# Optimization experiments

Measured on AMD Instinct MI355X. Metric: run time of the kernel, lower is better.

## Reference

```python
import jax, jax.numpy as jnp
import numpy as np

HEADS = 16


def fenwick_mask(T):
    # Boolean [T, T] mask: diagonal + Fenwick-tree lookback positions, causal.
    m = np.zeros((T, T), dtype=bool)
    for i in range(T):
        j = i + 1
        while j <= T:
            m[i, j - 1] = True
            j += j & -j
        step = 1
        while i - step >= 0:
            m[i, i - step] = True
            step *= 2
    m &= np.tril(np.ones((T, T), dtype=bool))  # causal
    return jnp.asarray(m)


def setup_inputs() -> dict:
    key = jax.random.key(0)
    ks = jax.random.split(key, 4)
    B, T, C = 2, 2048, 1024
    x = jax.random.normal(ks[0], (B, T, C), dtype=jnp.float32)
    W_qkv = jax.random.normal(ks[1], (C, 3 * C), dtype=jnp.float32) * (C ** -0.5)
    b_qkv = jnp.zeros((3 * C,), dtype=jnp.float32)
    W_proj = jax.random.normal(ks[2], (C, C), dtype=jnp.float32) * (C ** -0.5)
    b_proj = jnp.zeros((C,), dtype=jnp.float32)
    return {"x": x, "W_qkv": W_qkv, "b_qkv": b_qkv, "W_proj": W_proj, "b_proj": b_proj}


def reference(x, W_qkv, b_qkv, W_proj, b_proj):
    B, T, C = x.shape
    H = HEADS
    Dh = C // H
    scale = Dh ** -0.5
    qkv = (x @ W_qkv + b_qkv).reshape(B, T, 3, H, Dh)
    qkv = jnp.transpose(qkv, (2, 0, 3, 1, 4))  # [3, B, H, T, Dh]
    q, k, v = qkv[0], qkv[1], qkv[2]
    attn = jnp.einsum('bhtd,bhsd->bhts', q, k) * scale  # [B, H, T, T]
    mask = fenwick_mask(T)  # trace-time constant
    attn = jnp.where(mask[None, None], attn, -jnp.inf)
    attn = jax.nn.softmax(attn, axis=-1)
    out = jnp.einsum('bhts,bhsd->bhtd', attn, v)  # [B, H, T, Dh]
    out = jnp.transpose(out, (0, 2, 1, 3)).reshape(B, T, C)
    return out @ W_proj + b_proj
```

## Files before the change

kernel.cpp:

```cpp
#include <hip/hip_runtime.h>
#include <hip/hip_bf16.h>


typedef unsigned short ushort_t;
typedef __attribute__((ext_vector_type(8))) short s16x8;
typedef __attribute__((ext_vector_type(4))) float f32x4;

#define T_SEQ 2048
#define C_DIM 1024
#define HEADS 16

__device__ __forceinline__ ushort_t f2bf(float f) {
    union { float f; unsigned u; } v{f};
    unsigned r = v.u + 0x7FFFu + ((v.u >> 16) & 1u);
    return (ushort_t)(r >> 16);
}
__device__ __forceinline__ float bf2f(ushort_t u) {
    union { unsigned u; float f; } v{((unsigned)u) << 16};
    return v.f;
}

__device__ __forceinline__ void async16(const ushort_t* g, ushort_t* l) {
    __builtin_amdgcn_global_load_lds(
        (const __attribute__((address_space(1))) void*)g,
        (__attribute__((address_space(3))) void*)l, 16, 0, 0);
}

__global__ void prep(const float* __restrict__ x, ushort_t* __restrict__ xb,
                     const float* __restrict__ Wq, ushort_t* __restrict__ WqT,
                     const float* __restrict__ Wp, ushort_t* __restrict__ WpT) {
    const int bid = blockIdx.x;
    const int tid = threadIdx.x;
    if (bid < 4096) {
        const int i = bid * 256 + tid;
        float4 f = ((const float4*)x)[i];
        ushort4 o;
        o.x = f2bf(f.x); o.y = f2bf(f.y); o.z = f2bf(f.z); o.w = f2bf(f.w);
        ((ushort4*)xb)[i] = o;
    } else {
        __shared__ ushort_t tile[32][33];
        const float* W; ushort_t* WT; int N, nb, kb;
        if (bid < 7168) {
            const int tb = bid - 4096;
            W = Wq; WT = WqT; N = 3072; nb = (tb % 96) * 32; kb = (tb / 96) * 32;
        } else {
            const int tb = bid - 7168;
            W = Wp; WT = WpT; N = 1024; nb = (tb & 31) * 32; kb = (tb >> 5) * 32;
        }
        const int tx = tid & 31, ty = tid >> 5;
        #pragma unroll
        for (int i = ty; i < 32; i += 8)
            tile[i][tx] = f2bf(W[(size_t)(kb + i) * N + nb + tx]);
        __syncthreads();
        #pragma unroll
        for (int i = ty; i < 32; i += 8)
            WT[(size_t)(nb + i) * 1024 + kb + tx] = tile[tx][i];
    }
}

__global__ void gemm_qkv(const ushort_t* __restrict__ A, const ushort_t* __restrict__ BT,
                         const float* __restrict__ bias, ushort_t* __restrict__ C,
                         int N, int K) {
    __shared__ ushort_t lsA[128 * 64];
    __shared__ ushort_t lsB[128 * 64];

    const int tid  = threadIdx.x;
    const int wave = tid >> 6;
    const int lane = tid & 63;
    const int row0 = blockIdx.x * 128;
    const int col0 = blockIdx.y * 128;
    const int wr   = (wave >> 1) * 64;
    const int wc   = (wave & 1) * 64;
    const int lrow = lane & 15;
    const int quad = lane >> 4;
    const int crow = lane >> 3;
    const int gcol = ((lane & 7) ^ crow) * 8;
    const int d3   = lrow & 7;

    f32x4 acc[4][4] = {};

    for (int k0 = 0; k0 < K; k0 += 64) {
        #pragma unroll
        for (int it = 0; it < 4; ++it) {
            const int chunk = it * 4 + wave;
            const int r = chunk * 8 + crow;
            async16(A  + (size_t)(row0 + r) * K + (k0 + gcol), lsA + chunk * 512);
            async16(BT + (size_t)(col0 + r) * K + (k0 + gcol), lsB + chunk * 512);
        }
        __syncthreads();
        #pragma unroll
        for (int kk = 0; kk < 64; kk += 32) {
            const int g = (kk >> 3) + quad;
            const int slot = (g ^ d3) << 3;
            s16x8 af[4], bfr[4];
            #pragma unroll
            for (int i = 0; i < 4; ++i)
                af[i] = *(const s16x8*)(lsA + (wr + i * 16 + lrow) * 64 + slot);
            #pragma unroll
            for (int j = 0; j < 4; ++j)
                bfr[j] = *(const s16x8*)(lsB + (wc + j * 16 + lrow) * 64 + slot);
            #pragma unroll
            for (int i = 0; i < 4; ++i)
                #pragma unroll
                for (int j = 0; j < 4; ++j)
                    acc[i][j] = __builtin_amdgcn_mfma_f32_16x16x32_bf16(
                        af[i], bfr[j], acc[i][j], 0, 0, 0);
        }
        __syncthreads();
    }

    #pragma unroll
    for (int i = 0; i < 4; ++i) {
        #pragma unroll
        for (int j = 0; j < 4; ++j) {
            const int col = col0 + wc + j * 16 + lrow;
            const float bv = bias[col];
            #pragma unroll
            for (int r = 0; r < 4; ++r) {
                const int row = row0 + wr + i * 16 + quad * 4 + r;
                C[(size_t)row * N + col] = f2bf(acc[i][j][r] + bv);
            }
        }
    }
}

__global__ void gemm_proj(const ushort_t* __restrict__ A, const ushort_t* __restrict__ BT,
                          const float* __restrict__ bias, float* __restrict__ C,
                          int N, int K) {
    __shared__ ushort_t lsA[128 * 64];
    __shared__ ushort_t lsB[64 * 64];

    const int tid  = threadIdx.x;
    const int wave = tid >> 6;
    const int lane = tid & 63;
    const int row0 = blockIdx.x * 128;
    const int col0 = blockIdx.y * 64;
    const int lrow = lane & 15;
    const int quad = lane >> 4;
    const int crow = lane >> 3;
    const int gcol = ((lane & 7) ^ crow) * 8;
    const int d3   = lrow & 7;

    f32x4 acc[2][4] = {};

    for (int k0 = 0; k0 < K; k0 += 64) {
        #pragma unroll
        for (int it = 0; it < 4; ++it) {
            const int chunk = it * 4 + wave;
            const int r = chunk * 8 + crow;
            async16(A + (size_t)(row0 + r) * K + (k0 + gcol), lsA + chunk * 512);
        }
        #pragma unroll
        for (int it = 0; it < 2; ++it) {
            const int chunk = it * 4 + wave;
            const int r = chunk * 8 + crow;
            async16(BT + (size_t)(col0 + r) * K + (k0 + gcol), lsB + chunk * 512);
        }
        __syncthreads();
        #pragma unroll
        for (int kk = 0; kk < 64; kk += 32) {
            const int g = (kk >> 3) + quad;
            const int slot = (g ^ d3) << 3;
            s16x8 af[2], bfr[4];
            #pragma unroll
            for (int i = 0; i < 2; ++i)
                af[i] = *(const s16x8*)(lsA + (wave * 32 + i * 16 + lrow) * 64 + slot);
            #pragma unroll
            for (int j = 0; j < 4; ++j)
                bfr[j] = *(const s16x8*)(lsB + (j * 16 + lrow) * 64 + slot);
            #pragma unroll
            for (int i = 0; i < 2; ++i)
                #pragma unroll
                for (int j = 0; j < 4; ++j)
                    acc[i][j] = __builtin_amdgcn_mfma_f32_16x16x32_bf16(
                        af[i], bfr[j], acc[i][j], 0, 0, 0);
        }
        __syncthreads();
    }

    #pragma unroll
    for (int i = 0; i < 2; ++i) {
        #pragma unroll
        for (int j = 0; j < 4; ++j) {
            const int col = col0 + j * 16 + lrow;
            const float bv = bias[col];
            #pragma unroll
            for (int r = 0; r < 4; ++r) {
                const int row = row0 + wave * 32 + i * 16 + quad * 4 + r;
                C[(size_t)row * N + col] = acc[i][j][r] + bv;
            }
        }
    }
}

__global__ void fenwick_attn(const ushort_t* __restrict__ QKV, ushort_t* __restrict__ AO) {
    const int lane = threadIdx.x & 63;
    const int wid  = blockIdx.x * 4 + (threadIdx.x >> 6);
    const int tile = wid & 255;
    const int bh   = wid >> 8;
    const int h    = bh & (HEADS - 1);
    const int b    = bh >> 4;
    const int tl   = lane >> 3;
    const int g    = lane & 7;
    const int t    = tile * 8 + tl;

    const ushort_t* base = QKV + (size_t)(b * T_SEQ) * 3072 + h * 64 + g * 8;

    float qf[8];
    {
        s16x8 qv = *(const s16x8*)(base + (size_t)t * 3072);
        #pragma unroll
        for (int e = 0; e < 8; ++e) qf[e] = bf2f((ushort_t)qv[e]);
    }

    float logit[12];
    int   pos[12];
    float mx = -1e30f;
    #pragma unroll
    for (int s = 0; s < 12; ++s) {
        const int step = (s == 0) ? 0 : (1 << (s - 1));
        const bool act = (step <= t);
        const int p = act ? (t - step) : t;
        pos[s] = p;
        s16x8 kv = *(const s16x8*)(base + (size_t)p * 3072 + 1024);
        float l = 0.f;
        #pragma unroll
        for (int e = 0; e < 8; ++e) l = fmaf(qf[e], bf2f((ushort_t)kv[e]), l);
        l += __shfl_xor(l, 1, 64);
        l += __shfl_xor(l, 2, 64);
        l += __shfl_xor(l, 4, 64);
        l *= 0.125f;
        logit[s] = act ? l : -1e30f;
        mx = fmaxf(mx, logit[s]);
    }

    float denom = 0.f;
    float ov[8] = {};
    #pragma unroll
    for (int s = 0; s < 12; ++s) {
        const float w = __expf(logit[s] - mx);
        denom += w;
        s16x8 vv = *(const s16x8*)(base + (size_t)pos[s] * 3072 + 2048);
        #pragma unroll
        for (int e = 0; e < 8; ++e) ov[e] = fmaf(w, bf2f((ushort_t)vv[e]), ov[e]);
    }

    const float inv = 1.f / denom;
    s16x8 os;
    #pragma unroll
    for (int e = 0; e < 8; ++e) os[e] = (short)f2bf(ov[e] * inv);
    *(s16x8*)(AO + (size_t)(b * T_SEQ + t) * C_DIM + h * 64 + g * 8) = os;
}

extern "C" void kernel_launch(void* const* d_in, const int* in_sizes, int n_in,
                              void* d_out, int out_size, void* d_ws, size_t ws_size,
                              hipStream_t stream) {
    const float* x      = (const float*)d_in[0];
    const float* W_qkv  = (const float*)d_in[1];
    const float* b_qkv  = (const float*)d_in[2];
    const float* W_proj = (const float*)d_in[3];
    const float* b_proj = (const float*)d_in[4];
    float* out = (float*)d_out;

    char* ws = (char*)d_ws;
    ushort_t* xb     = (ushort_t*)(ws);
    ushort_t* WqkvT  = (ushort_t*)(ws + (size_t)8  * 1048576);
    ushort_t* QKVb   = (ushort_t*)(ws + (size_t)14 * 1048576);
    ushort_t* AO     = (ushort_t*)(ws + (size_t)38 * 1048576);
    ushort_t* WprojT = (ushort_t*)(ws + (size_t)46 * 1048576);

    prep<<<8192, 256, 0, stream>>>(x, xb, W_qkv, WqkvT, W_proj, WprojT);
    gemm_qkv<<<dim3(32, 24), 256, 0, stream>>>(xb, WqkvT, b_qkv, QKVb, 3072, 1024);
    fenwick_attn<<<2048, 256, 0, stream>>>(QKVb, AO);
    gemm_proj<<<dim3(32, 16), 256, 0, stream>>>(AO, WprojT, b_proj, out, 1024, 1024);
}
```

Before: 150.0 us.

## Rewrite QKV GEMM as 256x192 tile with double-buffered async LDS pipeline

Replaces the 128x128 single-buffered QKV GEMM with a 512-thread, 256x192 tile kernel. Global-to-LDS async loads for the next K tiles are interleaved with MFMA phases across two LDS buffers, using explicit vmcnt waits, barriers and raised priority during MFMA. This is meant to hide load latency and raise data reuse per tile. It uses 112 KB of LDS and a larger accumulator set, and gives a 256-block grid that may fill the CUs less evenly.

```diff
diff --git a/kernel.cpp b/kernel.cpp
--- a/kernel.cpp
+++ b/kernel.cpp
@@ -58,66 +58,110 @@
     }
 }
 
-__global__ void gemm_qkv(const ushort_t* __restrict__ A, const ushort_t* __restrict__ BT,
-                         const float* __restrict__ bias, ushort_t* __restrict__ C,
-                         int N, int K) {
-    __shared__ ushort_t lsA[128 * 64];
-    __shared__ ushort_t lsB[128 * 64];
+
+#define BAR()  do { __builtin_amdgcn_sched_barrier(0); __builtin_amdgcn_s_barrier(); \
+                    __builtin_amdgcn_sched_barrier(0); } while (0)
+#define WAIT_LGKM0() do { asm volatile("s_waitcnt lgkmcnt(0)" ::: "memory"); \
+                          __builtin_amdgcn_sched_barrier(0); } while (0)
+#define WAIT_VM(n)  asm volatile("s_waitcnt vmcnt(" #n ")" ::: "memory")
+
+#define SA(kt, u, dst) async16(Ag + (size_t)(u) * rstep + (size_t)(kt) * 64, \
+                               (dst) + (u) * 4096 + wave * 512)
+#define SB(kt, u, dst) async16(Bg + (size_t)(u) * rstep + (size_t)(kt) * 64, \
+                               (dst) + (u) * 4096 + wave * 512)
+
+#define LDA_FRAG(buf, i, kh) (*(const s16x8*)((buf) + ((wm << 7) + (i) * 16 + lrow) * 64 \
+                               + ((((kh) * 4 + quad) ^ d3) << 3)))
+#define LDB_FRAG(buf, j, kh) (*(const s16x8*)((buf) + (wn * 48 + (j) * 16 + lrow) * 64 \
+                               + ((((kh) * 4 + quad) ^ d3) << 3)))
+
+#define PHASE(lAb, lBb, Q, LOADB, STAGES, ENDWAIT)                              \
+  {                                                                             \
+    s16x8 af[2][2];                                                             \
+    _Pragma("unroll") for (int ii = 0; ii < 2; ++ii)                            \
+      _Pragma("unroll") for (int kh = 0; kh < 2; ++kh)                          \
+        af[ii][kh] = LDA_FRAG(lAb, 2 * (Q) + ii, kh);                           \
+    if (LOADB) {                                                                \
+      _Pragma("unroll") for (int j = 0; j < 3; ++j)                             \
+        _Pragma("unroll") for (int kh = 0; kh < 2; ++kh)                        \
+          bf[j][kh] = LDB_FRAG(lBb, j, kh);                                     \
+    }                                                                           \
+    STAGES;                                                                     \
+    BAR();                                                                      \
+    WAIT_LGKM0();                                                               \
+    __builtin_amdgcn_s_setprio(1);                                              \
+    _Pragma("unroll") for (int ii = 0; ii < 2; ++ii)                            \
+      _Pragma("unroll") for (int j = 0; j < 3; ++j)                             \
+        _Pragma("unroll") for (int kh = 0; kh < 2; ++kh)                        \
+          acc[2 * (Q) + ii][j] = __builtin_amdgcn_mfma_f32_16x16x32_bf16(       \
+              af[ii][kh], bf[j][kh], acc[2 * (Q) + ii][j], 0, 0, 0);            \
+    __builtin_amdgcn_s_setprio(0);                                              \
+    ENDWAIT;                                                                    \
+    BAR();                                                                      \
+  }
+
+__global__ __launch_bounds__(512, 2)
+void gemm_qkv(const ushort_t* __restrict__ A, const ushort_t* __restrict__ BT,
+              const float* __restrict__ bias, ushort_t* __restrict__ C,
+              int N, int K) {
+    __shared__ ushort_t lds[57344];
 
     const int tid  = threadIdx.x;
     const int wave = tid >> 6;
     const int lane = tid & 63;
-    const int row0 = blockIdx.x * 128;
-    const int col0 = blockIdx.y * 128;
-    const int wr   = (wave >> 1) * 64;
-    const int wc   = (wave & 1) * 64;
+    const int wm   = wave >> 2;
+    const int wn   = wave & 3;
     const int lrow = lane & 15;
     const int quad = lane >> 4;
+    const int d3   = lrow & 7;
     const int crow = lane >> 3;
-    const int gcol = ((lane & 7) ^ crow) * 8;
-    const int d3   = lrow & 7;
-
-    f32x4 acc[4][4] = {};
-
-    for (int k0 = 0; k0 < K; k0 += 64) {
-        #pragma unroll
-        for (int it = 0; it < 4; ++it) {
-            const int chunk = it * 4 + wave;
-            const int r = chunk * 8 + crow;
-            async16(A  + (size_t)(row0 + r) * K + (k0 + gcol), lsA + chunk * 512);
-            async16(BT + (size_t)(col0 + r) * K + (k0 + gcol), lsB + chunk * 512);
-        }
-        __syncthreads();
-        #pragma unroll
-        for (int kk = 0; kk < 64; kk += 32) {
-            const int g = (kk >> 3) + quad;
-            const int slot = (g ^ d3) << 3;
-            s16x8 af[4], bfr[4];
-            #pragma unroll
-            for (int i = 0; i < 4; ++i)
-                af[i] = *(const s16x8*)(lsA + (wr + i * 16 + lrow) * 64 + slot);
-            #pragma unroll
-            for (int j = 0; j < 4; ++j)
-                bfr[j] = *(const s16x8*)(lsB + (wc + j * 16 + lrow) * 64 + slot);
-            #pragma unroll
-            for (int i = 0; i < 4; ++i)
-                #pragma unroll
-                for (int j = 0; j < 4; ++j)
-                    acc[i][j] = __builtin_amdgcn_mfma_f32_16x16x32_bf16(
-                        af[i], bfr[j], acc[i][j], 0, 0, 0);
-        }
-        __syncthreads();
-    }
-
-    #pragma unroll
-    for (int i = 0; i < 4; ++i) {
-        #pragma unroll
-        for (int j = 0; j < 4; ++j) {
-            const int col = col0 + wc + j * 16 + lrow;
+    const int gcol = (((lane & 7) ^ crow) << 3);
+    const int row0 = blockIdx.x * 256;
+    const int col0 = blockIdx.y * 192;
+
+    ushort_t* const lA0 = lds;
+    ushort_t* const lB0 = lds + 16384;
+    ushort_t* const lA1 = lds + 28672;
+    ushort_t* const lB1 = lds + 45056;
+
+    const ushort_t* Ag = A  + (size_t)(row0 + wave * 8 + crow) * K + gcol;
+    const ushort_t* Bg = BT + (size_t)(col0 + wave * 8 + crow) * K + gcol;
+    const size_t rstep = (size_t)64 * K;
+
+    f32x4 acc[8][3] = {};
+    s16x8 bf[3][2];
+
+    SA(0, 0, lA0); SA(0, 1, lA0); SA(0, 2, lA0); SA(0, 3, lA0);
+    SB(0, 0, lB0); SB(0, 1, lB0); SB(0, 2, lB0);
+    SB(1, 0, lB1); SB(1, 1, lB1); SA(1, 0, lA1); SA(1, 2, lA1); SB(1, 2, lB1);
+    WAIT_VM(5);
+    BAR();
+
+    const int nt = K >> 6;
+    for (int t = 0; t < nt; t += 2) {
+        const bool s2 = (t + 2) < nt;
+        const bool s3 = (t + 3) < nt;
+        PHASE(lA0, lB0, 0, true,  { SA(t + 1, 1, lA1); SA(t + 1, 3, lA1); }, {});
+        PHASE(lA0, lB0, 1, false, { if (s2) { SB(t + 2, 0, lB0); SB(t + 2, 1, lB0); } }, {});
+        PHASE(lA0, lB0, 2, false, { if (s2) { SA(t + 2, 0, lA0); SA(t + 2, 2, lA0); } }, {});
+        PHASE(lA0, lB0, 3, false, { if (s2) { SB(t + 2, 2, lB0); } },
+              { if (s2) { WAIT_VM(5); } else { WAIT_VM(0); } });
+        PHASE(lA1, lB1, 0, true,  { if (s2) { SA(t + 2, 1, lA0); SA(t + 2, 3, lA0); } }, {});
+        PHASE(lA1, lB1, 1, false, { if (s3) { SB(t + 3, 0, lB1); SB(t + 3, 1, lB1); } }, {});
+        PHASE(lA1, lB1, 2, false, { if (s3) { SA(t + 3, 0, lA1); SA(t + 3, 2, lA1); } }, {});
+        PHASE(lA1, lB1, 3, false, { if (s3) { SB(t + 3, 2, lB1); } },
+              { WAIT_VM(5); });
+    }
+
+    #pragma unroll
+    for (int i = 0; i < 8; ++i) {
+        #pragma unroll
+        for (int j = 0; j < 3; ++j) {
+            const int col = col0 + wn * 48 + j * 16 + lrow;
             const float bv = bias[col];
             #pragma unroll
             for (int r = 0; r < 4; ++r) {
-                const int row = row0 + wr + i * 16 + quad * 4 + r;
+                const int row = row0 + (wm << 7) + i * 16 + quad * 4 + r;
                 C[(size_t)row * N + col] = f2bf(acc[i][j][r] + bv);
             }
         }
@@ -270,7 +314,7 @@
     ushort_t* WprojT = (ushort_t*)(ws + (size_t)46 * 1048576);
 
     prep<<<8192, 256, 0, stream>>>(x, xb, W_qkv, WqkvT, W_proj, WprojT);
-    gemm_qkv<<<dim3(32, 24), 256, 0, stream>>>(xb, WqkvT, b_qkv, QKVb, 3072, 1024);
+    gemm_qkv<<<dim3(16, 16), 512, 0, stream>>>(xb, WqkvT, b_qkv, QKVb, 3072, 1024);
     fenwick_attn<<<2048, 256, 0, stream>>>(QKVb, AO);
     gemm_proj<<<dim3(32, 16), 256, 0, stream>>>(AO, WprojT, b_proj, out, 1024, 1024);
 }
```

Measured after the change: 149.2 us. About the same (-0.6%).

## Add XCD-aware block swizzles, double-buffer and enlarge proj GEMM tiles

Applied to the files above, without the earlier changes.

Remaps block indices in both GEMMs and the attention kernel so that blocks landing on the same XCD (bid&7) share row or head data, improving L2 locality across the chiplets. The projection GEMM moves to 128x128 tiles with a double-buffered LDS pipeline that prefetches the next K-slice while computing the current one, and the QKV GEMM gets launch bounds. This trades fewer proj blocks (256), which may leave CUs underused, for better reuse and load/compute overlap.

```diff
diff --git a/kernel.cpp b/kernel.cpp
--- a/kernel.cpp
+++ b/kernel.cpp
@@ -58,17 +58,25 @@
     }
 }
 
-__global__ void gemm_qkv(const ushort_t* __restrict__ A, const ushort_t* __restrict__ BT,
-                         const float* __restrict__ bias, ushort_t* __restrict__ C,
-                         int N, int K) {
+__global__ __launch_bounds__(256, 4)
+void gemm_qkv(const ushort_t* __restrict__ A, const ushort_t* __restrict__ BT,
+              const float* __restrict__ bias, ushort_t* __restrict__ C,
+              int N, int K) {
     __shared__ ushort_t lsA[128 * 64];
     __shared__ ushort_t lsB[128 * 64];
 
     const int tid  = threadIdx.x;
     const int wave = tid >> 6;
     const int lane = tid & 63;
-    const int row0 = blockIdx.x * 128;
-    const int col0 = blockIdx.y * 128;
+
+    const int bid    = blockIdx.x;
+    const int xcd    = bid & 7;
+    const int q      = bid >> 3;
+    const int rowblk = ((xcd & 3) << 3) + (q & 7);
+    const int colblk = (xcd >> 2) * 12 + (q >> 3);
+    const int row0   = rowblk * 128;
+    const int col0   = colblk * 128;
+
     const int wr   = (wave >> 1) * 64;
     const int wc   = (wave & 1) * 64;
     const int lrow = lane & 15;
@@ -124,69 +132,78 @@
     }
 }
 
+#define PSTAGE(t, b) do {                                                        \
+    _Pragma("unroll") for (int it = 0; it < 4; ++it) {                           \
+        const int chunk = it * 4 + wave;                                         \
+        const int r = chunk * 8 + crow;                                          \
+        async16(A  + (size_t)(row0 + r) * K + ((t) * 64 + gcol), lsA[b] + chunk * 512); \
+        async16(BT + (size_t)(col0 + r) * K + ((t) * 64 + gcol), lsB[b] + chunk * 512); \
+    }                                                                            \
+} while (0)
+
 __global__ void gemm_proj(const ushort_t* __restrict__ A, const ushort_t* __restrict__ BT,
                           const float* __restrict__ bias, float* __restrict__ C,
                           int N, int K) {
-    __shared__ ushort_t lsA[128 * 64];
-    __shared__ ushort_t lsB[64 * 64];
+    __shared__ ushort_t lsA[2][128 * 64];
+    __shared__ ushort_t lsB[2][128 * 64];
 
     const int tid  = threadIdx.x;
     const int wave = tid >> 6;
     const int lane = tid & 63;
-    const int row0 = blockIdx.x * 128;
-    const int col0 = blockIdx.y * 64;
+
+    const int bid  = blockIdx.x;
+    const int xcd  = bid & 7;
+    const int q    = bid >> 3;
+    const int row0 = (xcd * 4 + (q & 3)) * 128;
+    const int col0 = (q >> 2) * 128;
+
+    const int wr   = (wave >> 1) * 64;
+    const int wc   = (wave & 1) * 64;
     const int lrow = lane & 15;
     const int quad = lane >> 4;
     const int crow = lane >> 3;
     const int gcol = ((lane & 7) ^ crow) * 8;
     const int d3   = lrow & 7;
 
-    f32x4 acc[2][4] = {};
-
-    for (int k0 = 0; k0 < K; k0 += 64) {
-        #pragma unroll
-        for (int it = 0; it < 4; ++it) {
-            const int chunk = it * 4 + wave;
-            const int r = chunk * 8 + crow;
-            async16(A + (size_t)(row0 + r) * K + (k0 + gcol), lsA + chunk * 512);
-        }
-        #pragma unroll
-        for (int it = 0; it < 2; ++it) {
-            const int chunk = it * 4 + wave;
-            const int r = chunk * 8 + crow;
-            async16(BT + (size_t)(col0 + r) * K + (k0 + gcol), lsB + chunk * 512);
-        }
-        __syncthreads();
+    f32x4 acc[4][4] = {};
+
+    const int nt = K >> 6;
+    int cur = 0;
+    PSTAGE(0, 0);
+    __syncthreads();
+    for (int t = 0; t < nt; ++t) {
+        if (t + 1 < nt) PSTAGE(t + 1, cur ^ 1);
         #pragma unroll
         for (int kk = 0; kk < 64; kk += 32) {
             const int g = (kk >> 3) + quad;
             const int slot = (g ^ d3) << 3;
-            s16x8 af[2], bfr[4];
-            #pragma unroll
-            for (int i = 0; i < 2; ++i)
-                af[i] = *(const s16x8*)(lsA + (wave * 32 + i * 16 + lrow) * 64 + slot);
+            s16x8 af[4], bfr[4];
+            #pragma unroll
+            for (int i = 0; i < 4; ++i)
+                af[i] = *(const s16x8*)(lsA[cur] + (wr + i * 16 + lrow) * 64 + slot);
             #pragma unroll
             for (int j = 0; j < 4; ++j)
-                bfr[j] = *(const s16x8*)(lsB + (j * 16 + lrow) * 64 + slot);
-            #pragma unroll
-            for (int i = 0; i < 2; ++i)
+                bfr[j] = *(const s16x8*)(lsB[cur] + (wc + j * 16 + lrow) * 64 + slot);
+            #pragma unroll
+            for (int i = 0; i < 4; ++i)
                 #pragma unroll
                 for (int j = 0; j < 4; ++j)
                     acc[i][j] = __builtin_amdgcn_mfma_f32_16x16x32_bf16(
                         af[i], bfr[j], acc[i][j], 0, 0, 0);
         }
         __syncthreads();
-    }
-
-    #pragma unroll
-    for (int i = 0; i < 2; ++i) {
+        cur ^= 1;
+    }
+
+    #pragma unroll
+    for (int i = 0; i < 4; ++i) {
         #pragma unroll
         for (int j = 0; j < 4; ++j) {
-            const int col = col0 + j * 16 + lrow;
+            const int col = col0 + wc + j * 16 + lrow;
             const float bv = bias[col];
             #pragma unroll
             for (int r = 0; r < 4; ++r) {
-                const int row = row0 + wave * 32 + i * 16 + quad * 4 + r;
+                const int row = row0 + wr + i * 16 + quad * 4 + r;
                 C[(size_t)row * N + col] = acc[i][j][r] + bv;
             }
         }
@@ -195,9 +212,11 @@
 
 __global__ void fenwick_attn(const ushort_t* __restrict__ QKV, ushort_t* __restrict__ AO) {
     const int lane = threadIdx.x & 63;
-    const int wid  = blockIdx.x * 4 + (threadIdx.x >> 6);
-    const int tile = wid & 255;
-    const int bh   = wid >> 8;
+    const int bid  = blockIdx.x;
+    const int xcd  = bid & 7;
+    const int q    = bid >> 3;
+    const int bh   = xcd + ((q >> 6) << 3);
+    const int tile = ((q & 63) << 2) + (threadIdx.x >> 6);
     const int h    = bh & (HEADS - 1);
     const int b    = bh >> 4;
     const int tl   = lane >> 3;
@@ -270,7 +289,7 @@
     ushort_t* WprojT = (ushort_t*)(ws + (size_t)46 * 1048576);
 
     prep<<<8192, 256, 0, stream>>>(x, xb, W_qkv, WqkvT, W_proj, WprojT);
-    gemm_qkv<<<dim3(32, 24), 256, 0, stream>>>(xb, WqkvT, b_qkv, QKVb, 3072, 1024);
+    gemm_qkv<<<768, 256, 0, stream>>>(xb, WqkvT, b_qkv, QKVb, 3072, 1024);
     fenwick_attn<<<2048, 256, 0, stream>>>(QKVb, AO);
-    gemm_proj<<<dim3(32, 16), 256, 0, stream>>>(AO, WprojT, b_proj, out, 1024, 1024);
-}
+    gemm_proj<<<256, 256, 0, stream>>>(AO, WprojT, b_proj, out, 1024, 1024);
+}
```

Measured after the change: 149.4 us. No clear change (-0.4%).
